# Optimization experiments

Hardware: AMD Instinct MI355X
Metric: run time of the kernel (lower is better)

The kernel has to match this reference:

```python
import jax, jax.numpy as jnp
import numpy as np

N = 100_000      # nodes
E = 1_600_000    # directed edges (before self-loops)
G = 128          # graphs in batch
IN = 32          # in_channels
HID = 32         # hidden_channels (per head)
HEADS = 4
SLOPE = 0.2      # GATConv leaky_relu negative_slope


def setup_inputs() -> dict:
    key = jax.random.key(0)
    ks = jax.random.split(key, 12)
    x = jax.random.normal(ks[0], (N, IN), jnp.float32)
    edge_index = jax.random.randint(ks[1], (2, E), 0, N)
    batch = jnp.sort(jax.random.randint(ks[2], (N,), 0, G))
    g = lambda k, sh: jax.random.normal(k, sh, jnp.float32) * (1.0 / np.sqrt(sh[0]))
    return {
        "x": x, "edge_index": edge_index, "batch": batch,
        # conv1: in -> heads*hid, concat
        "W1": g(ks[3], (IN, HEADS * HID)),
        "a_src1": jax.random.normal(ks[4], (HEADS, HID), jnp.float32) * 0.1,
        "a_dst1": jax.random.normal(ks[5], (HEADS, HID), jnp.float32) * 0.1,
        "b1": jnp.zeros((HEADS * HID,), jnp.float32),
        # conv2: heads*hid -> hid, heads=1, mean (concat=False)
        "W2": g(ks[6], (HEADS * HID, 1 * HID)),
        "a_src2": jax.random.normal(ks[7], (1, HID), jnp.float32) * 0.1,
        "a_dst2": jax.random.normal(ks[8], (1, HID), jnp.float32) * 0.1,
        "b2": jnp.zeros((HID,), jnp.float32),
        # classifier
        "Wc": g(ks[9], (HID, 1)),
        "bc": jnp.zeros((1,), jnp.float32),
    }


def _segment_softmax(e, seg, n):
    # e: [E', H]; softmax over edges sharing the same destination node
    m = jax.ops.segment_max(e, seg, num_segments=n)
    ex = jnp.exp(e - m[seg])
    den = jax.ops.segment_sum(ex, seg, num_segments=n)
    return ex / den[seg]


def _gat_layer(x, src, dst, W, a_src, a_dst, b, heads, ch, concat):
    n = x.shape[0]
    h = (x @ W).reshape(n, heads, ch)              # [N, H, C]
    e_src = jnp.sum(h * a_src, axis=-1)            # [N, H]
    e_dst = jnp.sum(h * a_dst, axis=-1)            # [N, H]
    e = jax.nn.leaky_relu(e_src[src] + e_dst[dst], SLOPE)   # [E', H]
    alpha = _segment_softmax(e, dst, n)            # [E', H]
    msg = h[src] * alpha[:, :, None]               # [E', H, C]
    out = jax.ops.segment_sum(msg, dst, num_segments=n)     # [N, H, C]
    out = out.reshape(n, heads * ch) if concat else out.mean(axis=1)
    return out + b


def reference(x, edge_index, batch, W1, a_src1, a_dst1, b1, W2, a_src2, a_dst2, b2, Wc, bc):
    n = x.shape[0]
    loops = jnp.arange(n, dtype=edge_index.dtype)  # GATConv add_self_loops=True
    src = jnp.concatenate([edge_index[0], loops])
    dst = jnp.concatenate([edge_index[1], loops])
    h = jax.nn.elu(_gat_layer(x, src, dst, W1, a_src1, a_dst1, b1, HEADS, HID, True))
    # dropout: eval mode -> identity
    h = jax.nn.elu(_gat_layer(h, src, dst, W2, a_src2, a_dst2, b2, 1, HID, False))
    # global_mean_pool over batch ids
    sums = jax.ops.segment_sum(h, batch, num_segments=G)
    cnt = jax.ops.segment_sum(jnp.ones((n, 1), h.dtype), batch, num_segments=G)
    pooled = sums / jnp.maximum(cnt, 1.0)
    return pooled @ Wc + bc                        # [G, 1]
```

## Files before the change

kernel.cpp:

```cpp
#include <hip/hip_runtime.h>
#include <math.h>

#define NT 100000
#define ET 1600000
#define GT 128
#define NBK 391
#define BSH 8
#define NBLK_A 256
#define CHUNK_A 6250

typedef float f4 __attribute__((ext_vector_type(4)));

__device__ __forceinline__ float lrelu(float v) { return v > 0.0f ? v : 0.2f * v; }
__device__ __forceinline__ float elu1(float v) { return v > 0.0f ? v : __expf(v) - 1.0f; }

__global__ __launch_bounds__(256) void k_histA(const int* __restrict__ dst, int* __restrict__ histA) {
  __shared__ int histL[NBK];
  int t = threadIdx.x, blk = blockIdx.x;
  for (int i = t; i < NBK; i += 256) histL[i] = 0;
  __syncthreads();
  int e0 = blk * CHUNK_A, e1 = min(ET, e0 + CHUNK_A);
  for (int e = e0 + t; e < e1; e += 256) atomicAdd(&histL[dst[e] >> BSH], 1);
  __syncthreads();
  for (int i = t; i < NBK; i += 256) histA[i * NBLK_A + blk] = histL[i];
}

__global__ __launch_bounds__(256) void k_scanB(int* __restrict__ histA, int* __restrict__ btot) {
  __shared__ int sh[256];
  int b = blockIdx.x, t = threadIdx.x;
  int v = histA[b * NBLK_A + t];
  sh[t] = v;
  __syncthreads();
  for (int off = 1; off < 256; off <<= 1) {
    int xv = (t >= off) ? sh[t - off] : 0;
    __syncthreads();
    sh[t] += xv;
    __syncthreads();
  }
  histA[b * NBLK_A + t] = sh[t] - v;
  if (t == 255) btot[b] = sh[255];
}

__global__ __launch_bounds__(512) void k_scanC(const int* __restrict__ btot, int* __restrict__ bbase) {
  __shared__ int sh[512];
  int t = threadIdx.x;
  int v = (t < NBK) ? btot[t] : 0;
  sh[t] = v;
  __syncthreads();
  for (int off = 1; off < 512; off <<= 1) {
    int xv = (t >= off) ? sh[t - off] : 0;
    __syncthreads();
    sh[t] += xv;
    __syncthreads();
  }
  if (t < NBK) bbase[t] = sh[t] - v;
  if (t == 0) bbase[NBK] = ET;
}

__global__ __launch_bounds__(256) void k_buck(const int* __restrict__ src, const int* __restrict__ dst,
                                              const int* __restrict__ histA, const int* __restrict__ bbase,
                                              unsigned int* __restrict__ ebuf) {
  __shared__ int cur[NBK];
  int t = threadIdx.x, blk = blockIdx.x;
  for (int i = t; i < NBK; i += 256) cur[i] = histA[i * NBLK_A + blk] + bbase[i];
  __syncthreads();
  int e0 = blk * CHUNK_A, e1 = min(ET, e0 + CHUNK_A);
  for (int e = e0 + t; e < e1; e += 256) {
    unsigned int s = (unsigned int)src[e];
    int d = dst[e];
    int pos = atomicAdd(&cur[d >> BSH], 1);
    ebuf[pos] = ((unsigned int)(d & 255) << 17) | s;
  }
}

__global__ __launch_bounds__(256) void k_fine(const unsigned int* __restrict__ ebuf, const int* __restrict__ bbase,
                                              int* __restrict__ rp, int* __restrict__ adj) {
  __shared__ int cnt[256];
  __shared__ int sh[256];
  __shared__ int cur[256];
  int b = blockIdx.x, t = threadIdx.x;
  int eb0 = bbase[b], eb1 = bbase[b + 1];
  cnt[t] = 0;
  __syncthreads();
  for (int e = eb0 + t; e < eb1; e += 256) atomicAdd(&cnt[ebuf[e] >> 17], 1);
  __syncthreads();
  int v = cnt[t];
  sh[t] = v;
  __syncthreads();
  for (int off = 1; off < 256; off <<= 1) {
    int xv = (t >= off) ? sh[t - off] : 0;
    __syncthreads();
    sh[t] += xv;
    __syncthreads();
  }
  int start = eb0 + sh[t] - v;
  cur[t] = start;
  int node = (b << BSH) + t;
  if (node < NT) rp[node] = start;
  if (node == NT - 1) rp[NT] = ET;
  __syncthreads();
  for (int e = eb0 + t; e < eb1; e += 256) {
    unsigned int p = ebuf[e];
    int pos = atomicAdd(&cur[p >> 17], 1);
    adj[pos] = (int)(p & 0x1FFFFu);
  }
}

__global__ void k_prep(const float* __restrict__ W1, const float* __restrict__ as1,
                       const float* __restrict__ ad1, float* __restrict__ AB) {
  int t = threadIdx.x;
  int k = t >> 3, j = t & 7;
  const float* a = (j < 4) ? as1 : ad1;
  int h = j & 3;
  float s = 0.0f;
  for (int c = 0; c < 32; ++c) s += W1[k * 128 + h * 32 + c] * a[h * 32 + c];
  AB[t] = s;
}

__global__ __launch_bounds__(256) void k_att1(const float* __restrict__ x, const float* __restrict__ AB,
                                              float* __restrict__ es, float* __restrict__ ed) {
  __shared__ float xsh[32 * 33];
  __shared__ float absh[256];
  int t = threadIdx.x;
  int n0 = blockIdx.x * 32;
  absh[t] = AB[t];
  for (int i = t; i < 1024; i += 256) {
    int ln = i >> 5, k = i & 31;
    int node = n0 + ln;
    xsh[ln * 33 + k] = (node < NT) ? x[node * 32 + k] : 0.0f;
  }
  __syncthreads();
  int ln = t >> 3, j = t & 7;
  int node = n0 + ln;
  if (node < NT) {
    float s = 0.0f;
#pragma unroll
    for (int k = 0; k < 32; ++k) s += xsh[ln * 33 + k] * absh[k * 8 + j];
    if (j < 4) es[node * 4 + j] = s;
    else ed[node * 4 + (j - 4)] = s;
  }
}

__global__ __launch_bounds__(256) void k_agg1g(
    const int* __restrict__ rp, const int* __restrict__ adj,
    const float* __restrict__ es, const float* __restrict__ ed,
    const float* __restrict__ x, float* __restrict__ y) {
  __shared__ int sbuf[8][34];
  __shared__ f4 wbufv[8][34];
  int t = threadIdx.x;
  int wv = t >> 6, l = t & 63;
  int g = l >> 5, j = l & 31;
  int ns = wv * 2 + g;
  int n = blockIdx.x * 8 + ns;
  if (n >= NT) return;
  const f4* es4 = (const f4*)es;
  int rs = rp[n], re = rp[n + 1];
  int deg = re - rs;
  f4 edn = ((const f4*)ed)[n];
  f4 esn = es4[n];
  float sv[4];
#pragma unroll
  for (int h = 0; h < 4; ++h) sv[h] = __expf(lrelu(esn[h] + edn[h]));
  int eg2 = j >> 3, q = j & 7;
  f4 a0 = {0,0,0,0}, a1 = {0,0,0,0}, a2 = {0,0,0,0}, a3 = {0,0,0,0};

  if (deg <= 32) {
    float ex[4] = {0.0f, 0.0f, 0.0f, 0.0f};
    if (j < deg) {
      int s = adj[rs + j];
      sbuf[ns][j] = s;
      f4 ev = es4[s];
#pragma unroll
      for (int h = 0; h < 4; ++h) ex[h] = __expf(lrelu(ev[h] + edn[h]));
    }
    float d[4] = {ex[0], ex[1], ex[2], ex[3]};
#pragma unroll
    for (int off = 1; off <= 16; off <<= 1)
#pragma unroll
      for (int h = 0; h < 4; ++h) d[h] += __shfl_xor(d[h], off);
    float inv[4];
#pragma unroll
    for (int h = 0; h < 4; ++h) inv[h] = 1.0f / (d[h] + sv[h]);
    if (j < deg) {
      f4 w4;
#pragma unroll
      for (int h = 0; h < 4; ++h) w4[h] = ex[h] * inv[h];
      wbufv[ns][j] = w4;
    }
    if (j == 0) {
      sbuf[ns][deg] = n;
      f4 w4;
#pragma unroll
      for (int h = 0; h < 4; ++h) w4[h] = sv[h] * inv[h];
      wbufv[ns][deg] = w4;
    }
    __builtin_amdgcn_wave_barrier();
    for (int e0 = eg2; e0 <= deg; e0 += 16) {
#pragma unroll
      for (int i = 0; i < 4; ++i) {
        int e = e0 + i * 4;
        if (e <= deg) {
          f4 xv = *(const f4*)&x[sbuf[ns][e] * 32 + 4 * q];
          f4 w4 = wbufv[ns][e];
          a0 += w4.x * xv; a1 += w4.y * xv; a2 += w4.z * xv; a3 += w4.w * xv;
        }
      }
    }
  } else {
    float d[4] = {0.0f, 0.0f, 0.0f, 0.0f};
    for (int jj = rs + j; jj < re; jj += 32) {
      f4 ev = es4[adj[jj]];
#pragma unroll
      for (int h = 0; h < 4; ++h) d[h] += __expf(lrelu(ev[h] + edn[h]));
    }
#pragma unroll
    for (int off = 1; off <= 16; off <<= 1)
#pragma unroll
      for (int h = 0; h < 4; ++h) d[h] += __shfl_xor(d[h], off);
    float inv[4];
#pragma unroll
    for (int h = 0; h < 4; ++h) inv[h] = 1.0f / (d[h] + sv[h]);
    for (int base = rs; base < re; base += 32) {
      int cnt = min(32, re - base);
      if (j < cnt) {
        int s = adj[base + j];
        sbuf[ns][j] = s;
        f4 ev = es4[s];
        f4 w4;
#pragma unroll
        for (int h = 0; h < 4; ++h) w4[h] = __expf(lrelu(ev[h] + edn[h])) * inv[h];
        wbufv[ns][j] = w4;
      }
      __builtin_amdgcn_wave_barrier();
      for (int e = eg2; e < cnt; e += 4) {
        f4 xv = *(const f4*)&x[sbuf[ns][e] * 32 + 4 * q];
        f4 w4 = wbufv[ns][e];
        a0 += w4.x * xv; a1 += w4.y * xv; a2 += w4.z * xv; a3 += w4.w * xv;
      }
      __builtin_amdgcn_wave_barrier();
    }
    if (eg2 == 0) {
      f4 xv = *(const f4*)&x[n * 32 + 4 * q];
      a0 += sv[0] * inv[0] * xv; a1 += sv[1] * inv[1] * xv;
      a2 += sv[2] * inv[2] * xv; a3 += sv[3] * inv[3] * xv;
    }
  }

#pragma unroll
  for (int off = 8; off <= 16; off <<= 1) {
#pragma unroll
    for (int cc = 0; cc < 4; ++cc) {
      a0[cc] += __shfl_xor(a0[cc], off);
      a1[cc] += __shfl_xor(a1[cc], off);
      a2[cc] += __shfl_xor(a2[cc], off);
      a3[cc] += __shfl_xor(a3[cc], off);
    }
  }
  if (eg2 == 0) {
    *(f4*)&y[n * 128 + 0 * 32 + 4 * q] = a0;
    *(f4*)&y[n * 128 + 1 * 32 + 4 * q] = a1;
    *(f4*)&y[n * 128 + 2 * 32 + 4 * q] = a2;
    *(f4*)&y[n * 128 + 3 * 32 + 4 * q] = a3;
  }
}

__global__ __launch_bounds__(256) void k_mv2(
    const float* __restrict__ y,
    const float* __restrict__ W1, const float* __restrict__ b1,
    const float* __restrict__ W2,
    const float* __restrict__ as2, const float* __restrict__ ad2,
    float* __restrict__ h2, float* __restrict__ es2, float* __restrict__ ed2) {
  __shared__ float ysh[128][33];
  __shared__ float osh[128][33];
  __shared__ float psh[32][37];
  int t = threadIdx.x;
  int n0 = blockIdx.x * 32;
  for (int it = t; it < 4096; it += 256) {
    int nd = it >> 7, c = it & 127;
    ysh[c][nd] = y[(n0 + nd) * 128 + c];
  }
  __syncthreads();

  int nd = t & 31, cq = t >> 5;
  int h = cq >> 1;
  f4 o4[4];
#pragma unroll
  for (int i = 0; i < 4; ++i) o4[i] = *(const f4*)&b1[cq * 16 + 4 * i];
#pragma unroll 4
  for (int k = 0; k < 32; ++k) {
    float yv = ysh[h * 32 + k][nd];
#pragma unroll
    for (int i = 0; i < 4; ++i) {
      f4 wv = *(const f4*)&W1[k * 128 + cq * 16 + 4 * i];
      o4[i] += yv * wv;
    }
  }
#pragma unroll
  for (int i = 0; i < 4; ++i) {
#pragma unroll
    for (int cc = 0; cc < 4; ++cc) {
      int c = cq * 16 + 4 * i + cc;
      osh[c][nd] = elu1(o4[i][cc]);
    }
  }
  __syncthreads();

  f4 p = {0, 0, 0, 0};
#pragma unroll 8
  for (int k = 0; k < 128; ++k) {
    float ov = osh[k][nd];
    p += ov * *(const f4*)&W2[k * 32 + cq * 4];
  }
  *(f4*)&psh[nd][cq * 4] = p;
  __syncthreads();

  {
    int nd2 = t >> 3, i8 = t & 7;
    f4 pv = *(const f4*)&psh[nd2][i8 * 4];
    *(f4*)&h2[(n0 + nd2) * 32 + i8 * 4] = pv;
  }
  if (t < 32) {
    float ps = 0.0f, pd = 0.0f;
#pragma unroll 8
    for (int c = 0; c < 32; ++c) {
      float pv = psh[t][c];
      ps += pv * as2[c];
      pd += pv * ad2[c];
    }
    es2[n0 + t] = ps;
    ed2[n0 + t] = pd;
  }
}

__global__ __launch_bounds__(256) void k_agg2(const int* __restrict__ rp, const int* __restrict__ adj,
                                              const float* __restrict__ es, const float* __restrict__ ed,
                                              const float* __restrict__ h, const float* __restrict__ b2,
                                              const float* __restrict__ Wc, float* __restrict__ z) {
  __shared__ int sbuf[8][34];
  __shared__ float wsh[8][34];
  int t = threadIdx.x;
  int wv = t >> 6, l = t & 63;
  int g = l >> 5, j = l & 31;
  int ns = wv * 2 + g;
  int n = blockIdx.x * 8 + ns;
  if (n >= NT) return;
  int rs = rp[n], re = rp[n + 1];
  int deg = re - rs;
  float edn = ed[n];
  float sv = __expf(lrelu(es[n] + edn));
  int eg2 = j >> 3, q = j & 7;
  f4 acc = {0,0,0,0};

  if (deg <= 32) {
    float ex = 0.0f;
    if (j < deg) {
      int s = adj[rs + j];
      sbuf[ns][j] = s;
      ex = __expf(lrelu(es[s] + edn));
    }
    float d = ex;
#pragma unroll
    for (int off = 1; off <= 16; off <<= 1) d += __shfl_xor(d, off);
    float inv = 1.0f / (d + sv);
    if (j < deg) wsh[ns][j] = ex * inv;
    if (j == 0) { sbuf[ns][deg] = n; wsh[ns][deg] = sv * inv; }
    __builtin_amdgcn_wave_barrier();
    for (int e0 = eg2; e0 <= deg; e0 += 16) {
#pragma unroll
      for (int i = 0; i < 4; ++i) {
        int e = e0 + i * 4;
        if (e <= deg) {
          acc += wsh[ns][e] * *(const f4*)&h[sbuf[ns][e] * 32 + 4 * q];
        }
      }
    }
  } else {
    float d = 0.0f;
    for (int jj = rs + j; jj < re; jj += 32) d += __expf(lrelu(es[adj[jj]] + edn));
#pragma unroll
    for (int off = 1; off <= 16; off <<= 1) d += __shfl_xor(d, off);
    float inv = 1.0f / (d + sv);
    for (int base = rs; base < re; base += 32) {
      int cnt = min(32, re - base);
      if (j < cnt) {
        int s = adj[base + j];
        sbuf[ns][j] = s;
        wsh[ns][j] = __expf(lrelu(es[s] + edn)) * inv;
      }
      __builtin_amdgcn_wave_barrier();
      for (int e = eg2; e < cnt; e += 4) {
        acc += wsh[ns][e] * *(const f4*)&h[sbuf[ns][e] * 32 + 4 * q];
      }
      __builtin_amdgcn_wave_barrier();
    }
    if (eg2 == 0) acc += sv * inv * *(const f4*)&h[n * 32 + 4 * q];
  }

#pragma unroll
  for (int off = 8; off <= 16; off <<= 1)
#pragma unroll
    for (int cc = 0; cc < 4; ++cc) acc[cc] += __shfl_xor(acc[cc], off);
  if (eg2 == 0) {
    f4 o = acc + *(const f4*)&b2[4 * q];
#pragma unroll
    for (int cc = 0; cc < 4; ++cc) o[cc] = elu1(o[cc]);
    f4 wc = *(const f4*)&Wc[4 * q];
    float zz = o.x * wc.x + o.y * wc.y + o.z * wc.z + o.w * wc.w;
#pragma unroll
    for (int off = 1; off <= 4; off <<= 1) zz += __shfl_xor(zz, off);
    if (q == 0) z[n] = zz;
  }
}

__global__ __launch_bounds__(256) void k_poolz(const float* __restrict__ z, const int* __restrict__ batch,
                                               const float* __restrict__ bc, float* __restrict__ out) {
  int g = blockIdx.x;
  int lo = 0, hi = NT;
  while (lo < hi) { int mid = (lo + hi) >> 1; if (batch[mid] < g) lo = mid + 1; else hi = mid; }
  int start = lo;
  hi = NT;
  while (lo < hi) { int mid = (lo + hi) >> 1; if (batch[mid] < g + 1) lo = mid + 1; else hi = mid; }
  int end = lo;

  int t = threadIdx.x;
  float s = 0.0f;
  for (int n = start + t; n < end; n += 256) s += z[n];
#pragma unroll
  for (int off = 1; off <= 32; off <<= 1) s += __shfl_xor(s, off);
  __shared__ float sh[4];
  if ((t & 63) == 0) sh[t >> 6] = s;
  __syncthreads();
  if (t == 0) {
    float tot = sh[0] + sh[1] + sh[2] + sh[3];
    float cnt = (float)(end - start);
    out[g] = tot / fmaxf(cnt, 1.0f) + bc[0];
  }
}

extern "C" void kernel_launch(void* const* d_in, const int* in_sizes, int n_in,
                              void* d_out, int out_size, void* d_ws, size_t ws_size,
                              hipStream_t stream) {
  const float* x = (const float*)d_in[0];
  const int* ei = (const int*)d_in[1];
  const int* src = ei;
  const int* dst = ei + ET;
  const int* batch = (const int*)d_in[2];
  const float* W1 = (const float*)d_in[3];
  const float* asrc1 = (const float*)d_in[4];
  const float* adst1 = (const float*)d_in[5];
  const float* b1 = (const float*)d_in[6];
  const float* W2 = (const float*)d_in[7];
  const float* asrc2 = (const float*)d_in[8];
  const float* adst2 = (const float*)d_in[9];
  const float* b2 = (const float*)d_in[10];
  const float* Wc = (const float*)d_in[11];
  const float* bc = (const float*)d_in[12];
  float* out = (float*)d_out;
  char* ws = (char*)d_ws;

  int* row_ptr = (int*)(ws + 0);
  int* histA = (int*)(ws + 400128);
  int* btot = (int*)(ws + 800512);
  int* bbase = (int*)(ws + 802112);
  float* AB = (float*)(ws + 803712);
  unsigned int* ebuf = (unsigned int*)(ws + 804736);
  int* adj = (int*)(ws + 7204736);
  float* es1 = (float*)(ws + 13604736);
  float* ed1 = (float*)(ws + 15204736);
  float* es2 = (float*)(ws + 16804736);
  float* ed2 = (float*)(ws + 17204736);
  float* h2 = (float*)(ws + 17604736);
  float* z = (float*)(ws + 30404736);
  float* y = (float*)(ws + 30804736);

  k_histA<<<NBLK_A, 256, 0, stream>>>(dst, histA);
  k_scanB<<<NBK, 256, 0, stream>>>(histA, btot);
  k_scanC<<<1, 512, 0, stream>>>(btot, bbase);
  k_buck<<<NBLK_A, 256, 0, stream>>>(src, dst, histA, bbase, ebuf);
  k_fine<<<NBK, 256, 0, stream>>>(ebuf, bbase, row_ptr, adj);

  k_prep<<<1, 256, 0, stream>>>(W1, asrc1, adst1, AB);
  k_att1<<<(NT + 31) / 32, 256, 0, stream>>>(x, AB, es1, ed1);

  k_agg1g<<<(NT + 7) / 8, 256, 0, stream>>>(row_ptr, adj, es1, ed1, x, y);

  k_mv2<<<NT / 32, 256, 0, stream>>>(y, W1, b1, W2, asrc2, adst2, h2, es2, ed2);

  k_agg2<<<(NT + 7) / 8, 256, 0, stream>>>(row_ptr, adj, es2, ed2, h2, b2, Wc, z);

  k_poolz<<<GT, 256, 0, stream>>>(z, batch, bc, out);
}
```

Measured before the change: 261.2 us.

## Split dense layer transform into two register-tiled kernels with shared-memory weights

The fused per-node W1-then-W2 transform kernel is split into two kernels. k_mv1 applies W1, the bias and ELU, and writes a new 100000x128 intermediate buffer. k_mv2 reads that buffer and applies W2 plus the attention projections. Both stage the weights in shared memory and compute a 4-node by multi-channel register tile per thread, so weight and activation loads are reused across outputs. The cost is an extra launch and a 51 MB round trip through global memory for the intermediate.

```diff
diff --git a/kernel.cpp b/kernel.cpp
--- a/kernel.cpp
+++ b/kernel.cpp
@@ -10,6 +10,7 @@
 #define CHUNK_A 6250
 
 typedef float f4 __attribute__((ext_vector_type(4)));
+typedef float f2 __attribute__((ext_vector_type(2)));
 
 __device__ __forceinline__ float lrelu(float v) { return v > 0.0f ? v : 0.2f * v; }
 __device__ __forceinline__ float elu1(float v) { return v > 0.0f ? v : __expf(v) - 1.0f; }
@@ -264,71 +265,116 @@
   }
 }
 
-__global__ __launch_bounds__(256) void k_mv2(
+__global__ __launch_bounds__(256) void k_mv1(
     const float* __restrict__ y,
     const float* __restrict__ W1, const float* __restrict__ b1,
+    float* __restrict__ o_out) {
+  __shared__ float W1sh[4096];
+  __shared__ float b1sh[128];
+  __shared__ float ysh[32 * 129];
+  int t = threadIdx.x;
+  int n0 = blockIdx.x * 32;
+  for (int i = t; i < 4096; i += 256) W1sh[i] = W1[i];
+  if (t < 128) b1sh[t] = b1[t];
+  for (int i = t; i < 1024; i += 256) {
+    int nd = i >> 5, q = i & 31;
+    f4 v = *(const f4*)&y[(n0 + nd) * 128 + q * 4];
+    ysh[nd * 129 + q * 4 + 0] = v.x;
+    ysh[nd * 129 + q * 4 + 1] = v.y;
+    ysh[nd * 129 + q * 4 + 2] = v.z;
+    ysh[nd * 129 + q * 4 + 3] = v.w;
+  }
+  __syncthreads();
+
+  int m4 = t & 7, c4 = t >> 3;
+  int h = c4 >> 3;
+  f4 acc0 = {0,0,0,0}, acc1 = {0,0,0,0}, acc2 = {0,0,0,0}, acc3 = {0,0,0,0};
+  int ybase = h * 32;
+#pragma unroll 8
+  for (int k = 0; k < 32; ++k) {
+    f4 wv = *(const f4*)&W1sh[k * 128 + c4 * 4];
+    float y0 = ysh[(m4 * 4 + 0) * 129 + ybase + k];
+    float y1 = ysh[(m4 * 4 + 1) * 129 + ybase + k];
+    float y2 = ysh[(m4 * 4 + 2) * 129 + ybase + k];
+    float y3 = ysh[(m4 * 4 + 3) * 129 + ybase + k];
+    acc0 += y0 * wv; acc1 += y1 * wv; acc2 += y2 * wv; acc3 += y3 * wv;
+  }
+  f4 bb = *(const f4*)&b1sh[c4 * 4];
+  acc0 += bb; acc1 += bb; acc2 += bb; acc3 += bb;
+#pragma unroll
+  for (int cc = 0; cc < 4; ++cc) {
+    acc0[cc] = elu1(acc0[cc]); acc1[cc] = elu1(acc1[cc]);
+    acc2[cc] = elu1(acc2[cc]); acc3[cc] = elu1(acc3[cc]);
+  }
+  int obase = (n0 + m4 * 4) * 128 + c4 * 4;
+  *(f4*)&o_out[obase + 0 * 128] = acc0;
+  *(f4*)&o_out[obase + 1 * 128] = acc1;
+  *(f4*)&o_out[obase + 2 * 128] = acc2;
+  *(f4*)&o_out[obase + 3 * 128] = acc3;
+}
+
+__global__ __launch_bounds__(256) void k_mv2(
+    const float* __restrict__ o_in,
     const float* __restrict__ W2,
     const float* __restrict__ as2, const float* __restrict__ ad2,
     float* __restrict__ h2, float* __restrict__ es2, float* __restrict__ ed2) {
-  __shared__ float ysh[128][33];
-  __shared__ float osh[128][33];
-  __shared__ float psh[32][37];
-  int t = threadIdx.x;
-  int n0 = blockIdx.x * 32;
-  for (int it = t; it < 4096; it += 256) {
-    int nd = it >> 7, c = it & 127;
-    ysh[c][nd] = y[(n0 + nd) * 128 + c];
-  }
-  __syncthreads();
-
-  int nd = t & 31, cq = t >> 5;
-  int h = cq >> 1;
-  f4 o4[4];
-#pragma unroll
-  for (int i = 0; i < 4; ++i) o4[i] = *(const f4*)&b1[cq * 16 + 4 * i];
-#pragma unroll 4
-  for (int k = 0; k < 32; ++k) {
-    float yv = ysh[h * 32 + k][nd];
+  __shared__ float W2sh[4096];
+  __shared__ float osh[64 * 129];
+  int t = threadIdx.x;
+  int n0 = blockIdx.x * 64;
+  for (int i = t; i < 4096; i += 256) W2sh[i] = W2[i];
+  for (int i = t; i < 8192; i += 256) {
+    int nd = i >> 7, k = i & 127;
+    int node = n0 + nd;
+    osh[nd * 129 + k] = (node < NT) ? o_in[node * 128 + k] : 0.0f;
+  }
+  __syncthreads();
+
+  int m4 = t & 15, c2 = t >> 4;
+  f2 acc0 = {0,0}, acc1 = {0,0}, acc2 = {0,0}, acc3 = {0,0};
+#pragma unroll 16
+  for (int k = 0; k < 128; ++k) {
+    f2 wv = *(const f2*)&W2sh[k * 32 + c2 * 2];
+    float o0 = osh[(m4 * 4 + 0) * 129 + k];
+    float o1 = osh[(m4 * 4 + 1) * 129 + k];
+    float o2 = osh[(m4 * 4 + 2) * 129 + k];
+    float o3 = osh[(m4 * 4 + 3) * 129 + k];
+    acc0 += o0 * wv; acc1 += o1 * wv; acc2 += o2 * wv; acc3 += o3 * wv;
+  }
+  __syncthreads();
+  float* psh = osh;
+  {
+    int c0 = c2 * 2;
+    psh[(m4 * 4 + 0) * 33 + c0] = acc0.x; psh[(m4 * 4 + 0) * 33 + c0 + 1] = acc0.y;
+    psh[(m4 * 4 + 1) * 33 + c0] = acc1.x; psh[(m4 * 4 + 1) * 33 + c0 + 1] = acc1.y;
+    psh[(m4 * 4 + 2) * 33 + c0] = acc2.x; psh[(m4 * 4 + 2) * 33 + c0 + 1] = acc2.y;
+    psh[(m4 * 4 + 3) * 33 + c0] = acc3.x; psh[(m4 * 4 + 3) * 33 + c0 + 1] = acc3.y;
+  }
+  {
+    int c0 = c2 * 2;
 #pragma unroll
     for (int i = 0; i < 4; ++i) {
-      f4 wv = *(const f4*)&W1[k * 128 + cq * 16 + 4 * i];
-      o4[i] += yv * wv;
-    }
-  }
-#pragma unroll
-  for (int i = 0; i < 4; ++i) {
-#pragma unroll
-    for (int cc = 0; cc < 4; ++cc) {
-      int c = cq * 16 + 4 * i + cc;
-      osh[c][nd] = elu1(o4[i][cc]);
-    }
-  }
-  __syncthreads();
-
-  f4 p = {0, 0, 0, 0};
+      int node = n0 + m4 * 4 + i;
+      if (node < NT) {
+        f2 v = (i == 0) ? acc0 : (i == 1) ? acc1 : (i == 2) ? acc2 : acc3;
+        *(f2*)&h2[node * 32 + c0] = v;
+      }
+    }
+  }
+  __syncthreads();
+  if (t < 64) {
+    int node = n0 + t;
+    if (node < NT) {
+      float ps = 0.0f, pd = 0.0f;
 #pragma unroll 8
-  for (int k = 0; k < 128; ++k) {
-    float ov = osh[k][nd];
-    p += ov * *(const f4*)&W2[k * 32 + cq * 4];
-  }
-  *(f4*)&psh[nd][cq * 4] = p;
-  __syncthreads();
-
-  {
-    int nd2 = t >> 3, i8 = t & 7;
-    f4 pv = *(const f4*)&psh[nd2][i8 * 4];
-    *(f4*)&h2[(n0 + nd2) * 32 + i8 * 4] = pv;
-  }
-  if (t < 32) {
-    float ps = 0.0f, pd = 0.0f;
-#pragma unroll 8
-    for (int c = 0; c < 32; ++c) {
-      float pv = psh[t][c];
-      ps += pv * as2[c];
-      pd += pv * ad2[c];
-    }
-    es2[n0 + t] = ps;
-    ed2[n0 + t] = pd;
+      for (int c = 0; c < 32; ++c) {
+        float pv = psh[t * 33 + c];
+        ps += pv * as2[c];
+        pd += pv * ad2[c];
+      }
+      es2[node] = ps;
+      ed2[node] = pd;
+    }
   }
 }
 
@@ -472,6 +518,7 @@
   float* h2 = (float*)(ws + 17604736);
   float* z = (float*)(ws + 30404736);
   float* y = (float*)(ws + 30804736);
+  float* o_buf = (float*)(ws + 82004736);
 
   k_histA<<<NBLK_A, 256, 0, stream>>>(dst, histA);
   k_scanB<<<NBK, 256, 0, stream>>>(histA, btot);
@@ -484,7 +531,8 @@
 
   k_agg1g<<<(NT + 7) / 8, 256, 0, stream>>>(row_ptr, adj, es1, ed1, x, y);
 
-  k_mv2<<<NT / 32, 256, 0, stream>>>(y, W1, b1, W2, asrc2, adst2, h2, es2, ed2);
+  k_mv1<<<NT / 32, 256, 0, stream>>>(y, W1, b1, o_buf);
+  k_mv2<<<(NT + 63) / 64, 256, 0, stream>>>(o_buf, W2, asrc2, adst2, h2, es2, ed2);
 
   k_agg2<<<(NT + 7) / 8, 256, 0, stream>>>(row_ptr, adj, es2, ed2, h2, b2, Wc, z);
 
```

New measurement: 242.2 us. 7.3% less time.
